# Kernel optimization log

Hardware: AMD Instinct MI355X
Metric: run time of the kernel (lower is better)

The kernel has to match this reference:

```python
import jax, jax.numpy as jnp
import numpy as np

BN_EPS = 1e-5
SQ_EPS = 1e-7
NUM_SAMPLES = 4
NUM_CHILD = 8
DIM_CHILD = 8
NUM_PARENT = 8
DIM_PARENT = 16
ROUTING_ITERS = 3
OFFSET_SCALE = 1.0


def squash(x, axis=-1):
    sq = jnp.sum(x * x, axis=axis, keepdims=True)
    return (sq / (1.0 + sq)) * x / jnp.sqrt(sq + SQ_EPS)


def bilinear_sample(feat, grid):
    # feat: [B,C,H,W], grid: [B,H,W,2] in [-1,1], align_corners=True, zeros padding
    B, C, H, W = feat.shape
    x = (grid[..., 0] + 1.0) * 0.5 * (W - 1)
    y = (grid[..., 1] + 1.0) * 0.5 * (H - 1)
    x0 = jnp.floor(x); y0 = jnp.floor(y)
    x1 = x0 + 1.0; y1 = y0 + 1.0
    wx1 = x - x0; wx0 = 1.0 - wx1
    wy1 = y - y0; wy0 = 1.0 - wy1
    featf = feat.reshape(B, C, H * W)

    def gather(xi, yi):
        valid = (xi >= 0) & (xi <= W - 1) & (yi >= 0) & (yi <= H - 1)
        xc = jnp.clip(xi, 0, W - 1).astype(jnp.int32)
        yc = jnp.clip(yi, 0, H - 1).astype(jnp.int32)
        idx = (yc * W + xc).reshape(B, 1, H * W)
        v = jnp.take_along_axis(featf, idx, axis=2).reshape(B, C, H, W)
        return v * valid[:, None].astype(feat.dtype)

    out = (gather(x0, y0) * (wx0 * wy0)[:, None]
           + gather(x1, y0) * (wx1 * wy0)[:, None]
           + gather(x0, y1) * (wx0 * wy1)[:, None]
           + gather(x1, y1) * (wx1 * wy1)[:, None])
    return out


def setup_inputs() -> dict:
    key = jax.random.key(0)
    ks = jax.random.split(key, 8)
    B, C, H, W = 8, 256, 32, 32
    caps_ch = NUM_CHILD * DIM_CHILD  # 64
    return {
        "x": jax.random.normal(ks[0], (B, C, H, W), jnp.float32),
        "primary_w": jax.random.normal(ks[1], (caps_ch, C), jnp.float32) * 0.05,
        "bn_gamma": jnp.ones((caps_ch,), jnp.float32),
        "bn_beta": jnp.zeros((caps_ch,), jnp.float32),
        "bn_mean": jax.random.normal(ks[2], (caps_ch,), jnp.float32) * 0.1,
        "bn_var": jax.random.uniform(ks[3], (caps_ch,), jnp.float32, 0.5, 1.5),
        "offset_w": jax.random.normal(ks[4], (2 * NUM_SAMPLES, C, 3, 3), jnp.float32) * 0.01,
        "offset_b": jnp.zeros((2 * NUM_SAMPLES,), jnp.float32),
        "routing_W": jax.random.normal(ks[5], (NUM_SAMPLES * NUM_CHILD, NUM_PARENT, DIM_PARENT, DIM_CHILD), jnp.float32) * 0.01,
    }


def reference(x, primary_w, bn_gamma, bn_beta, bn_mean, bn_var, offset_w, offset_b, routing_W):
    B, C, H, W = x.shape
    # --- PrimaryCaps: 1x1 conv + BN(inference) + SiLU + squash over capsule dim ---
    p = jnp.einsum('bchw,oc->bohw', x, primary_w)
    p = (p - bn_mean[None, :, None, None]) / jnp.sqrt(bn_var + BN_EPS)[None, :, None, None]
    p = p * bn_gamma[None, :, None, None] + bn_beta[None, :, None, None]
    p = jax.nn.silu(p)
    child = p.reshape(B, NUM_CHILD, DIM_CHILD, H, W)
    child = squash(child, axis=2)
    child_flat = child.reshape(B, NUM_CHILD * DIM_CHILD, H, W)

    # --- Offset conv 3x3, SAME padding ---
    off = jax.lax.conv_general_dilated(x, offset_w, (1, 1), 'SAME',
                                       dimension_numbers=('NCHW', 'OIHW', 'NCHW'))
    off = off + offset_b[None, :, None, None]
    off = off.reshape(B, NUM_SAMPLES, 2, H, W)
    off = jnp.tanh(off) * OFFSET_SCALE
    scale = jnp.array([max(W - 1, 1) / 2.0, max(H - 1, 1) / 2.0], x.dtype).reshape(1, 1, 2, 1, 1)
    off = off / scale

    ys = jnp.linspace(-1.0, 1.0, H, dtype=x.dtype)
    xs = jnp.linspace(-1.0, 1.0, W, dtype=x.dtype)
    yy, xx = jnp.meshgrid(ys, xs, indexing='ij')
    base = jnp.stack((xx, yy), axis=-1)  # [H,W,2]
    grids = base[None, None] + jnp.transpose(off, (0, 1, 3, 4, 2))  # [B,S,H,W,2]

    sampled = jax.vmap(lambda g: bilinear_sample(child_flat, g),
                       in_axes=1, out_axes=1)(grids)  # [B,S,caps_ch,H,W]
    sampled = sampled.reshape(B, NUM_SAMPLES, NUM_CHILD, DIM_CHILD, H, W)
    sampled = jnp.transpose(sampled, (0, 4, 5, 1, 2, 3))  # [B,H,W,S,NC,DC]
    sampled = sampled.reshape(B * H * W, NUM_SAMPLES * NUM_CHILD, DIM_CHILD)

    # --- Dynamic routing ---
    # u_hat: [M, N_in, N_out, D_out]
    u_hat = jnp.einsum('nodi,mni->mnod', routing_W, sampled)
    M = u_hat.shape[0]
    b = jnp.zeros((M, NUM_SAMPLES * NUM_CHILD, NUM_PARENT), x.dtype)
    v = None
    for it in range(ROUTING_ITERS):
        c = jax.nn.softmax(b, axis=-1)
        s = jnp.einsum('mno,mnod->mod', c, u_hat)
        v = squash(s, axis=-1)
        if it < ROUTING_ITERS - 1:
            b = b + jnp.einsum('mnod,mod->mno', u_hat, v)

    routed = v.reshape(B, H, W, NUM_PARENT, DIM_PARENT)
    out = jnp.transpose(routed, (0, 3, 4, 1, 2)).reshape(B, NUM_PARENT * DIM_PARENT, H, W)
    return out
```

## Files before the change

kernel.cpp:

```cpp
#include <hip/hip_runtime.h>
#include <math.h>

#define HW 1024
#define Hd 32
#define Wd 32
#define Bn 8
#define Cc 256

typedef _Float16 half2_t __attribute__((ext_vector_type(2)));
union F2H { float f; half2_t h; };

static __device__ __forceinline__ float dot2(half2_t a, half2_t b, float c) {
#if __has_builtin(__builtin_amdgcn_fdot2)
    return __builtin_amdgcn_fdot2(a, b, c, false);
#else
    return c + (float)a.x * (float)b.x + (float)a.y * (float)b.y;
#endif
}

template<int CTRL>
static __device__ __forceinline__ float dppx(float v) {
    union { float f; int i; } a, r;
    a.f = v;
    r.i = __builtin_amdgcn_update_dpp(0, a.i, CTRL, 0xF, 0xF, true);
    return r.f;
}

__global__ __launch_bounds__(256) void kTP(const float* __restrict__ x,
        const float* __restrict__ ow, const float* __restrict__ rw,
        float* __restrict__ xt, float* __restrict__ wt2,
        _Float16* __restrict__ wth) {
    __shared__ float tile[64][65];
    int bid = blockIdx.x;
    if (bid < 512) {
        int b = bid >> 6, ct = (bid >> 4) & 3, ht = bid & 15;
        int c0 = ct * 64, hw0 = ht * 64;
        int tr = threadIdx.x >> 6, tc = threadIdx.x & 63;
        const float* xb = x + ((size_t)b * 256 + c0) * 1024 + hw0;
        #pragma unroll
        for (int k = 0; k < 16; ++k) {
            int c = tr + k * 4;
            tile[c][tc] = xb[(size_t)c * 1024 + tc];
        }
        __syncthreads();
        float* xo = xt + ((size_t)b * 1024 + hw0) * 256 + c0;
        #pragma unroll
        for (int k = 0; k < 16; ++k) {
            int hwl = tr + k * 4;
            xo[(size_t)hwl * 256 + tc] = tile[tc][hwl];
        }
    } else if (bid < 584) {
        int t = (bid - 512) * 256 + threadIdx.x;
        int c = t & 255, oc = (t >> 8) & 7, tap = t >> 11;
        wt2[t] = ow[(oc * 256 + c) * 9 + tap];
    } else {
        int t = (bid - 584) * 256 + threadIdx.x;
        int i = t & 7, l = (t >> 3) & 63, j = t >> 9;
        int n = (l & 3) | ((l >> 1) & 0x1C);
        int half = (l >> 2) & 1;
        int o = j >> 4, d = j & 15;
        wth[t] = (_Float16)rw[n * 1024 + half * 512 + o * 128 + d * 8 + i];
    }
}

__global__ __launch_bounds__(256, 3) void kAB(const float* __restrict__ xt,
        const float* __restrict__ pw, const float* __restrict__ gamma,
        const float* __restrict__ beta, const float* __restrict__ mean,
        const float* __restrict__ var, const float* __restrict__ wt2,
        const float* __restrict__ ob, float* __restrict__ child_t,
        float* __restrict__ grids) {
    __shared__ float wl[16384];
    int wid = threadIdx.x >> 6, lane = threadIdx.x & 63;

    if (blockIdx.x < 512) {
        {
            const float4* pw4 = reinterpret_cast<const float4*>(pw);
            #pragma unroll
            for (int k = 0; k < 16; ++k) {
                int f = k * 256 + threadIdx.x;
                float4 v = pw4[f];
                int o = f >> 6, c4 = f & 63;
                *reinterpret_cast<float4*>(
                    wl + c4 * 256 + (((o ^ c4) & 63) << 2)) = v;
            }
        }
        __syncthreads();
        int o = lane;
        float scale = gamma[o] * rsqrtf(var[o] + 1e-5f);
        float mn = mean[o], bt = beta[o];
        const float4* wl4 = reinterpret_cast<const float4*>(wl);
        #pragma unroll
        for (int pp = 0; pp < 4; pp += 2) {
            int m0 = (blockIdx.x * 4 + wid) * 4 + pp;
            const float4* xa = reinterpret_cast<const float4*>(xt + (size_t)m0 * 256);
            const float4* xb = reinterpret_cast<const float4*>(xt + (size_t)(m0 + 1) * 256);
            float a0 = 0.f, a1 = 0.f;
            #pragma unroll 8
            for (int c4 = 0; c4 < 64; ++c4) {
                float4 wv = wl4[c4 * 64 + (lane ^ (c4 & 63))];
                float4 v0 = xa[c4], v1 = xb[c4];
                a0 += wv.x * v0.x + wv.y * v0.y + wv.z * v0.z + wv.w * v0.w;
                a1 += wv.x * v1.x + wv.y * v1.y + wv.z * v1.z + wv.w * v1.w;
            }
            #pragma unroll
            for (int e = 0; e < 2; ++e) {
                float acc = e ? a1 : a0;
                float t = (acc - mn) * scale + bt;
                float s = t / (1.f + expf(-t));
                float sq = s * s;
                sq += __shfl_xor(sq, 1);
                sq += __shfl_xor(sq, 2);
                sq += __shfl_xor(sq, 4);
                float f = (sq / (1.f + sq)) * rsqrtf(sq + 1e-7f);
                child_t[(size_t)(m0 + e) * 64 + o] = s * f;
            }
        }
        return;
    }

    {
        const float4* wt24 = reinterpret_cast<const float4*>(wt2);
        float4* wl4w = reinterpret_cast<float4*>(wl);
        #pragma unroll
        for (int k = 0; k < 16; ++k)
            wl4w[k * 256 + threadIdx.x] = wt24[k * 256 + threadIdx.x];
    }
    __syncthreads();

    int m0 = ((blockIdx.x - 512) * 4 + wid) * 4;
    int b = m0 >> 10, hw0 = m0 & 1023;
    int yy = hw0 >> 5, xx0 = hw0 & 31;
    const float* xb = xt + (size_t)b * HW * 256;

    float acc[4][8];
    #pragma unroll
    for (int px = 0; px < 4; ++px)
        #pragma unroll
        for (int oc = 0; oc < 8; ++oc) acc[px][oc] = 0.f;

    #pragma unroll
    for (int tap = 0; tap < 9; ++tap) {
        int ky = tap / 3 - 1, kx = tap % 3 - 1;
        int yq = yy + ky;
        bool vy = (yq >= 0) && (yq <= Hd - 1);
        float4 xv[4];
        #pragma unroll
        for (int px = 0; px < 4; ++px) {
            int xq = xx0 + px + kx;
            bool ok = vy && (xq >= 0) && (xq <= Wd - 1);
            float4 z; z.x = z.y = z.z = z.w = 0.f;
            xv[px] = ok ? *reinterpret_cast<const float4*>(
                              xb + (size_t)(yq * Wd + xq) * 256 + lane * 4)
                        : z;
        }
        #pragma unroll
        for (int oc = 0; oc < 8; ++oc) {
            float4 wv = (tap < 8)
                ? *reinterpret_cast<const float4*>(wl + (tap * 8 + oc) * 256 + lane * 4)
                : *reinterpret_cast<const float4*>(wt2 + (8 * 8 + oc) * 256 + lane * 4);
            #pragma unroll
            for (int px = 0; px < 4; ++px)
                acc[px][oc] += xv[px].x * wv.x + xv[px].y * wv.y +
                               xv[px].z * wv.z + xv[px].w * wv.w;
        }
    }

    int l0 = lane & 1, l1 = (lane >> 1) & 1;
    int o2 = (lane >> 2) & 1, o3 = (lane >> 3) & 1, o4 = (lane >> 4) & 1;
    float y1[2][8];
    #pragma unroll
    for (int ph = 0; ph < 2; ++ph)
        #pragma unroll
        for (int oc = 0; oc < 8; ++oc) {
            float keep = l0 ? acc[(ph << 1) | 1][oc] : acc[(ph << 1) | 0][oc];
            float send = l0 ? acc[(ph << 1) | 0][oc] : acc[(ph << 1) | 1][oc];
            y1[ph][oc] = keep + dppx<0xB1>(send);
        }
    float y2[8];
    #pragma unroll
    for (int oc = 0; oc < 8; ++oc) {
        float keep = l1 ? y1[1][oc] : y1[0][oc];
        float send = l1 ? y1[0][oc] : y1[1][oc];
        y2[oc] = keep + dppx<0x4E>(send);
    }
    float z4[4];
    #pragma unroll
    for (int oh = 0; oh < 4; ++oh) {
        float keep = o2 ? y2[(oh << 1) | 1] : y2[(oh << 1) | 0];
        float send = o2 ? y2[(oh << 1) | 0] : y2[(oh << 1) | 1];
        z4[oh] = keep + __shfl_xor(send, 4);
    }
    float w2[2];
    #pragma unroll
    for (int oh = 0; oh < 2; ++oh) {
        float keep = o3 ? z4[(oh << 1) | 1] : z4[(oh << 1) | 0];
        float send = o3 ? z4[(oh << 1) | 0] : z4[(oh << 1) | 1];
        w2[oh] = keep + dppx<0x128>(send);
    }
    {
        float keep = o4 ? w2[1] : w2[0];
        float send = o4 ? w2[0] : w2[1];
        float s = keep + __shfl_xor(send, 16);
        s += __shfl_xor(s, 32);
        if (lane < 32) {
            int px = lane & 3, oc = (lane >> 2) & 7;
            float t = tanhf(s + ob[oc]);
            int coord = oc & 1, si = oc >> 1;
            int xx = xx0 + px;
            float base = coord ? (-1.f + yy * (2.f / 31.f))
                               : (-1.f + xx * (2.f / 31.f));
            grids[(size_t)(m0 + px) * 8 + si * 2 + coord] =
                base + t * (1.f / 15.5f);
        }
    }
}

__global__ __launch_bounds__(64, 3) void kD(const float* __restrict__ child_t,
        const float* __restrict__ grids, const _Float16* __restrict__ wth,
        float* __restrict__ out) {
    __shared__ float vband[128];
    int lane = threadIdx.x & 63;
    int m = blockIdx.x;
    int b = m >> 10, hw = m & 1023;
    int n = (lane & 3) | ((lane >> 1) & 0x1C);
    int half = (lane >> 2) & 1;
    int si = n >> 3, ch = n & 7;
    int dsl = (n & 1) * 8 + ((n >> 1) & 1) * 4 + ((n >> 2) & 1) * 2 + ((n >> 3) & 1);

    float gx = grids[m * 8 + si * 2 + 0];
    float gy = grids[m * 8 + si * 2 + 1];
    float xf = (gx + 1.f) * 0.5f * 31.f;
    float yf = (gy + 1.f) * 0.5f * 31.f;
    float x0 = floorf(xf), y0 = floorf(yf);
    float wx1 = xf - x0, wx0 = 1.f - wx1;
    float wy1 = yf - y0, wy0 = 1.f - wy1;
    float sf[8] = {0.f, 0.f, 0.f, 0.f, 0.f, 0.f, 0.f, 0.f};
    const float* cb = child_t + (size_t)b * HW * 64 + ch * 8;
    #pragma unroll
    for (int cy = 0; cy < 2; ++cy) {
        float yq = y0 + (float)cy;
        bool vy = (yq >= 0.f) && (yq <= 31.f);
        float wy = cy ? wy1 : wy0;
        #pragma unroll
        for (int cx = 0; cx < 2; ++cx) {
            float xq = x0 + (float)cx;
            bool ok = vy && (xq >= 0.f) && (xq <= 31.f);
            if (!ok) continue;
            float w = wy * (cx ? wx1 : wx0);
            const float* cp = cb + (size_t)((int)yq * Wd + (int)xq) * 64;
            float4 v0 = *reinterpret_cast<const float4*>(cp);
            float4 v1 = *reinterpret_cast<const float4*>(cp + 4);
            sf[0] += w * v0.x; sf[1] += w * v0.y;
            sf[2] += w * v0.z; sf[3] += w * v0.w;
            sf[4] += w * v1.x; sf[5] += w * v1.y;
            sf[6] += w * v1.z; sf[7] += w * v1.w;
        }
    }
    half2_t sh0 = {(_Float16)sf[0], (_Float16)sf[1]};
    half2_t sh1 = {(_Float16)sf[2], (_Float16)sf[3]};
    half2_t sh2 = {(_Float16)sf[4], (_Float16)sf[5]};
    half2_t sh3 = {(_Float16)sf[6], (_Float16)sf[7]};

    float u[4][16];
    const float4* wt4 = reinterpret_cast<const float4*>(wth);
    #pragma unroll
    for (int o = 0; o < 4; ++o) {
        #pragma unroll
        for (int d = 0; d < 16; ++d) {
            float4 wv = wt4[(o * 16 + d) * 64 + lane];
            F2H a0, a1, a2, a3;
            a0.f = wv.x; a1.f = wv.y; a2.f = wv.z; a3.f = wv.w;
            float acc = dot2(a0.h, sh0, 0.f);
            acc = dot2(a1.h, sh1, acc);
            acc = dot2(a2.h, sh2, acc);
            acc = dot2(a3.h, sh3, acc);
            u[o][d] = acc;
        }
    }

    float bl[4] = {0.f, 0.f, 0.f, 0.f};
    #pragma unroll
    for (int it = 0; it < 3; ++it) {
        float ex[4], rs;
        if (it == 0) {
            ex[0] = ex[1] = ex[2] = ex[3] = 1.f;
            rs = 0.125f;
        } else {
            float mx = fmaxf(fmaxf(bl[0], bl[1]), fmaxf(bl[2], bl[3]));
            mx = fmaxf(mx, __shfl_xor(mx, 4));
            float ssum = 0.f;
            #pragma unroll
            for (int k = 0; k < 4; ++k) { ex[k] = expf(bl[k] - mx); ssum += ex[k]; }
            ssum += __shfl_xor(ssum, 4);
            rs = 1.f / ssum;
        }

        float sval[4];
        #pragma unroll
        for (int o = 0; o < 4; ++o) {
            float cc = ex[o] * rs;
            float y[8];
            #pragma unroll
            for (int d = 0; d < 8; ++d) {
                float t = (n & 1) ? cc * u[o][d] : cc * u[o][d + 8];
                float k = (n & 1) ? cc * u[o][d + 8] : cc * u[o][d];
                y[d] = k + dppx<0xB1>(t);
            }
            float z[4];
            #pragma unroll
            for (int d = 0; d < 4; ++d) {
                float t = (n & 2) ? y[d] : y[d + 4];
                float k = (n & 2) ? y[d + 4] : y[d];
                z[d] = k + dppx<0x4E>(t);
            }
            float w2[2];
            #pragma unroll
            for (int d = 0; d < 2; ++d) {
                float t = (n & 4) ? z[d] : z[d + 2];
                float k = (n & 4) ? z[d + 2] : z[d];
                w2[d] = k + dppx<0x128>(t);
            }
            float t4 = (n & 8) ? w2[0] : w2[1];
            float k4 = (n & 8) ? w2[1] : w2[0];
            float s1 = k4 + __shfl_xor(t4, 16);
            s1 += __shfl_xor(s1, 32);
            sval[o] = s1;
        }
        #pragma unroll
        for (int o = 0; o < 4; ++o) {
            float q = sval[o] * sval[o];
            q += dppx<0xB1>(q);
            q += dppx<0x4E>(q);
            q += dppx<0x128>(q);
            q += __shfl_xor(q, 16);
            float f = (q / (1.f + q)) / sqrtf(q + 1e-7f);
            if ((lane & 32) == 0)
                vband[(half * 4 + o) * 16 + dsl] = sval[o] * f;
        }
        if (it < 2) {
            #pragma unroll
            for (int o = 0; o < 4; ++o) {
                const float4* vr = reinterpret_cast<const float4*>(
                    vband + (half * 4 + o) * 16);
                float4 v0 = vr[0], v1 = vr[1], v2 = vr[2], v3 = vr[3];
                float agg = u[o][0] * v0.x + u[o][1] * v0.y +
                            u[o][2] * v0.z + u[o][3] * v0.w +
                            u[o][4] * v1.x + u[o][5] * v1.y +
                            u[o][6] * v1.z + u[o][7] * v1.w +
                            u[o][8] * v2.x + u[o][9] * v2.y +
                            u[o][10] * v2.z + u[o][11] * v2.w +
                            u[o][12] * v3.x + u[o][13] * v3.y +
                            u[o][14] * v3.z + u[o][15] * v3.w;
                bl[o] += agg;
            }
        } else {
            int o_own = lane >> 4;
            int och = half * 4 + o_own;
            int d0 = ((lane & 3) | ((lane >> 1) & 4)) * 2;
            float va = vband[och * 16 + d0 + 0];
            float vb = vband[och * 16 + d0 + 1];
            float* op = out + ((size_t)b * 128 + och * 16) * HW + hw;
            op[(size_t)(d0 + 0) * HW] = va;
            op[(size_t)(d0 + 1) * HW] = vb;
        }
    }
}

extern "C" void kernel_launch(void* const* d_in, const int* in_sizes, int n_in,
                              void* d_out, int out_size, void* d_ws, size_t ws_size,
                              hipStream_t stream) {
    const float* x     = (const float*)d_in[0];
    const float* pw    = (const float*)d_in[1];
    const float* gamma = (const float*)d_in[2];
    const float* beta  = (const float*)d_in[3];
    const float* mean  = (const float*)d_in[4];
    const float* var   = (const float*)d_in[5];
    const float* ow    = (const float*)d_in[6];
    const float* ob    = (const float*)d_in[7];
    const float* rw    = (const float*)d_in[8];
    float* out = (float*)d_out;
    char* ws = (char*)d_ws;
    float*     child_t = (float*)ws;
    float*     grids   = (float*)(ws + 2097152);
    _Float16*  wth     = (_Float16*)(ws + 2359296);
    float*     wt2     = (float*)(ws + 2424832);
    float*     xt      = (float*)(ws + 2498560);

    hipLaunchKernelGGL(kTP, dim3(712), dim3(256), 0, stream,
                       x, ow, rw, xt, wt2, wth);
    hipLaunchKernelGGL(kAB, dim3(1024), dim3(256), 0, stream,
                       xt, pw, gamma, beta, mean, var, wt2, ob,
                       child_t, grids);
    hipLaunchKernelGGL(kD, dim3(8192), dim3(64), 0, stream,
                       child_t, grids, wth, out);
}
```

Measured before the change: 85.52 us.

## Restructure routing kernel to four waves over two pixels with one parent per lane

The routing kernel now runs 256-thread blocks that each handle two pixels. Every wave owns two parent capsules, and each lane holds u_hat for one child and one parent across both pixels. Bilinear samples are computed once per block and shared through LDS. The softmax over parents is exchanged through an LDS table, which needs extra block barriers. The aim is to reuse each routing-weight load across two pixels and cut per-lane register pressure, paid for with more __syncthreads per routing iteration and a reordered weight layout.

```diff
diff --git a/kernel.cpp b/kernel.cpp
--- a/kernel.cpp
+++ b/kernel.cpp
@@ -55,11 +55,10 @@
         wt2[t] = ow[(oc * 256 + c) * 9 + tap];
     } else {
         int t = (bid - 584) * 256 + threadIdx.x;
-        int i = t & 7, l = (t >> 3) & 63, j = t >> 9;
-        int n = (l & 3) | ((l >> 1) & 0x1C);
-        int half = (l >> 2) & 1;
-        int o = j >> 4, d = j & 15;
-        wth[t] = (_Float16)rw[n * 1024 + half * 512 + o * 128 + d * 8 + i];
+        int i = t & 7, l = (t >> 3) & 63, j = (t >> 9) & 15, w = t >> 13;
+        int n = l & 31, s = l >> 5;
+        int o = 2 * w + s;
+        wth[t] = (_Float16)rw[n * 1024 + o * 128 + j * 8 + i];
     }
 }
 
@@ -215,95 +214,139 @@
     }
 }
 
-__global__ __launch_bounds__(64, 3) void kD(const float* __restrict__ child_t,
+__global__ __launch_bounds__(256, 2) void kD(const float* __restrict__ child_t,
         const float* __restrict__ grids, const _Float16* __restrict__ wth,
         float* __restrict__ out) {
-    __shared__ float vband[128];
-    int lane = threadIdx.x & 63;
-    int m = blockIdx.x;
-    int b = m >> 10, hw = m & 1023;
-    int n = (lane & 3) | ((lane >> 1) & 0x1C);
-    int half = (lane >> 2) & 1;
-    int si = n >> 3, ch = n & 7;
+    __shared__ float smp[2][32][8];
+    __shared__ float btab[2][32][8];
+    __shared__ float vband[2][8][16];
+    int tid = threadIdx.x;
+    int w = tid >> 6, lane = tid & 63;
+    int n = lane & 31, sh = lane >> 5;
+    int o_own = 2 * w + sh;
     int dsl = (n & 1) * 8 + ((n >> 1) & 1) * 4 + ((n >> 2) & 1) * 2 + ((n >> 3) & 1);
-
-    float gx = grids[m * 8 + si * 2 + 0];
-    float gy = grids[m * 8 + si * 2 + 1];
-    float xf = (gx + 1.f) * 0.5f * 31.f;
-    float yf = (gy + 1.f) * 0.5f * 31.f;
-    float x0 = floorf(xf), y0 = floorf(yf);
-    float wx1 = xf - x0, wx0 = 1.f - wx1;
-    float wy1 = yf - y0, wy0 = 1.f - wy1;
-    float sf[8] = {0.f, 0.f, 0.f, 0.f, 0.f, 0.f, 0.f, 0.f};
-    const float* cb = child_t + (size_t)b * HW * 64 + ch * 8;
-    #pragma unroll
-    for (int cy = 0; cy < 2; ++cy) {
-        float yq = y0 + (float)cy;
-        bool vy = (yq >= 0.f) && (yq <= 31.f);
-        float wy = cy ? wy1 : wy0;
-        #pragma unroll
-        for (int cx = 0; cx < 2; ++cx) {
-            float xq = x0 + (float)cx;
-            bool ok = vy && (xq >= 0.f) && (xq <= 31.f);
-            if (!ok) continue;
-            float w = wy * (cx ? wx1 : wx0);
-            const float* cp = cb + (size_t)((int)yq * Wd + (int)xq) * 64;
-            float4 v0 = *reinterpret_cast<const float4*>(cp);
-            float4 v1 = *reinterpret_cast<const float4*>(cp + 4);
-            sf[0] += w * v0.x; sf[1] += w * v0.y;
-            sf[2] += w * v0.z; sf[3] += w * v0.w;
-            sf[4] += w * v1.x; sf[5] += w * v1.y;
-            sf[6] += w * v1.z; sf[7] += w * v1.w;
-        }
-    }
-    half2_t sh0 = {(_Float16)sf[0], (_Float16)sf[1]};
-    half2_t sh1 = {(_Float16)sf[2], (_Float16)sf[3]};
-    half2_t sh2 = {(_Float16)sf[4], (_Float16)sf[5]};
-    half2_t sh3 = {(_Float16)sf[6], (_Float16)sf[7]};
-
-    float u[4][16];
-    const float4* wt4 = reinterpret_cast<const float4*>(wth);
-    #pragma unroll
-    for (int o = 0; o < 4; ++o) {
-        #pragma unroll
-        for (int d = 0; d < 16; ++d) {
-            float4 wv = wt4[(o * 16 + d) * 64 + lane];
-            F2H a0, a1, a2, a3;
-            a0.f = wv.x; a1.f = wv.y; a2.f = wv.z; a3.f = wv.w;
-            float acc = dot2(a0.h, sh0, 0.f);
-            acc = dot2(a1.h, sh1, acc);
-            acc = dot2(a2.h, sh2, acc);
-            acc = dot2(a3.h, sh3, acc);
-            u[o][d] = acc;
-        }
-    }
-
-    float bl[4] = {0.f, 0.f, 0.f, 0.f};
+    int mA = blockIdx.x * 2;
+    int bA_ = mA >> 10, hwA = mA & 1023;
+    int bB_ = (mA + 1) >> 10, hwB = (mA + 1) & 1023;
+
+    if (tid < 64) {
+        int px = tid >> 5, ns = tid & 31;
+        int sis = ns >> 3, chs = ns & 7;
+        int m = mA + px;
+        int b = m >> 10;
+        float gx = grids[m * 8 + sis * 2 + 0];
+        float gy = grids[m * 8 + sis * 2 + 1];
+        float xf = (gx + 1.f) * 0.5f * 31.f;
+        float yf = (gy + 1.f) * 0.5f * 31.f;
+        float x0 = floorf(xf), y0 = floorf(yf);
+        float wx1 = xf - x0, wx0 = 1.f - wx1;
+        float wy1 = yf - y0, wy0 = 1.f - wy1;
+        float sf[8] = {0.f, 0.f, 0.f, 0.f, 0.f, 0.f, 0.f, 0.f};
+        const float* cb = child_t + (size_t)b * HW * 64 + chs * 8;
+        #pragma unroll
+        for (int cy = 0; cy < 2; ++cy) {
+            float yq = y0 + (float)cy;
+            bool vy = (yq >= 0.f) && (yq <= 31.f);
+            float wy = cy ? wy1 : wy0;
+            #pragma unroll
+            for (int cx = 0; cx < 2; ++cx) {
+                float xq = x0 + (float)cx;
+                bool ok = vy && (xq >= 0.f) && (xq <= 31.f);
+                if (!ok) continue;
+                float wgt = wy * (cx ? wx1 : wx0);
+                const float* cp = cb + (size_t)((int)yq * Wd + (int)xq) * 64;
+                float4 v0 = *reinterpret_cast<const float4*>(cp);
+                float4 v1 = *reinterpret_cast<const float4*>(cp + 4);
+                sf[0] += wgt * v0.x; sf[1] += wgt * v0.y;
+                sf[2] += wgt * v0.z; sf[3] += wgt * v0.w;
+                sf[4] += wgt * v1.x; sf[5] += wgt * v1.y;
+                sf[6] += wgt * v1.z; sf[7] += wgt * v1.w;
+            }
+        }
+        float4 s0; s0.x = sf[0]; s0.y = sf[1]; s0.z = sf[2]; s0.w = sf[3];
+        float4 s1; s1.x = sf[4]; s1.y = sf[5]; s1.z = sf[6]; s1.w = sf[7];
+        reinterpret_cast<float4*>(&smp[px][ns][0])[0] = s0;
+        reinterpret_cast<float4*>(&smp[px][ns][0])[1] = s1;
+    }
+    __syncthreads();
+
+    half2_t sha[4], shb[4];
+    {
+        const float4* pa = reinterpret_cast<const float4*>(&smp[0][n][0]);
+        float4 a0 = pa[0], a1 = pa[1];
+        sha[0] = half2_t{(_Float16)a0.x, (_Float16)a0.y};
+        sha[1] = half2_t{(_Float16)a0.z, (_Float16)a0.w};
+        sha[2] = half2_t{(_Float16)a1.x, (_Float16)a1.y};
+        sha[3] = half2_t{(_Float16)a1.z, (_Float16)a1.w};
+        const float4* pb = reinterpret_cast<const float4*>(&smp[1][n][0]);
+        float4 b0 = pb[0], b1 = pb[1];
+        shb[0] = half2_t{(_Float16)b0.x, (_Float16)b0.y};
+        shb[1] = half2_t{(_Float16)b0.z, (_Float16)b0.w};
+        shb[2] = half2_t{(_Float16)b1.x, (_Float16)b1.y};
+        shb[3] = half2_t{(_Float16)b1.z, (_Float16)b1.w};
+    }
+
+    float ua[16], ub[16];
+    const float4* wt4 = reinterpret_cast<const float4*>(wth) + (size_t)w * 16 * 64 + lane;
+    #pragma unroll
+    for (int j = 0; j < 16; ++j) {
+        float4 wv = wt4[j * 64];
+        F2H a0, a1, a2, a3;
+        a0.f = wv.x; a1.f = wv.y; a2.f = wv.z; a3.f = wv.w;
+        float acc = dot2(a0.h, sha[0], 0.f);
+        acc = dot2(a1.h, sha[1], acc);
+        acc = dot2(a2.h, sha[2], acc);
+        acc = dot2(a3.h, sha[3], acc);
+        ua[j] = acc;
+        float accB = dot2(a0.h, shb[0], 0.f);
+        accB = dot2(a1.h, shb[1], accB);
+        accB = dot2(a2.h, shb[2], accB);
+        accB = dot2(a3.h, shb[3], accB);
+        ub[j] = accB;
+    }
+
+    float bA = 0.f, bB = 0.f;
     #pragma unroll
     for (int it = 0; it < 3; ++it) {
-        float ex[4], rs;
+        float cA, cB;
         if (it == 0) {
-            ex[0] = ex[1] = ex[2] = ex[3] = 1.f;
-            rs = 0.125f;
+            cA = 0.125f; cB = 0.125f;
         } else {
-            float mx = fmaxf(fmaxf(bl[0], bl[1]), fmaxf(bl[2], bl[3]));
-            mx = fmaxf(mx, __shfl_xor(mx, 4));
-            float ssum = 0.f;
-            #pragma unroll
-            for (int k = 0; k < 4; ++k) { ex[k] = expf(bl[k] - mx); ssum += ex[k]; }
-            ssum += __shfl_xor(ssum, 4);
-            rs = 1.f / ssum;
-        }
-
-        float sval[4];
-        #pragma unroll
-        for (int o = 0; o < 4; ++o) {
-            float cc = ex[o] * rs;
+            __syncthreads();
+            btab[0][n][o_own] = bA;
+            btab[1][n][o_own] = bB;
+            __syncthreads();
+            float4 qa0 = reinterpret_cast<const float4*>(&btab[0][n][0])[0];
+            float4 qa1 = reinterpret_cast<const float4*>(&btab[0][n][0])[1];
+            float4 qb0 = reinterpret_cast<const float4*>(&btab[1][n][0])[0];
+            float4 qb1 = reinterpret_cast<const float4*>(&btab[1][n][0])[1];
+            float mxA = fmaxf(fmaxf(fmaxf(qa0.x, qa0.y), fmaxf(qa0.z, qa0.w)),
+                              fmaxf(fmaxf(qa1.x, qa1.y), fmaxf(qa1.z, qa1.w)));
+            float esA = expf(qa0.x - mxA) + expf(qa0.y - mxA) +
+                        expf(qa0.z - mxA) + expf(qa0.w - mxA) +
+                        expf(qa1.x - mxA) + expf(qa1.y - mxA) +
+                        expf(qa1.z - mxA) + expf(qa1.w - mxA);
+            cA = expf(bA - mxA) / esA;
+            float mxB = fmaxf(fmaxf(fmaxf(qb0.x, qb0.y), fmaxf(qb0.z, qb0.w)),
+                              fmaxf(fmaxf(qb1.x, qb1.y), fmaxf(qb1.z, qb1.w)));
+            float esB = expf(qb0.x - mxB) + expf(qb0.y - mxB) +
+                        expf(qb0.z - mxB) + expf(qb0.w - mxB) +
+                        expf(qb1.x - mxB) + expf(qb1.y - mxB) +
+                        expf(qb1.z - mxB) + expf(qb1.w - mxB);
+            cB = expf(bB - mxB) / esB;
+        }
+
+        #pragma unroll
+        for (int px = 0; px < 2; ++px) {
+            float cc = px ? cB : cA;
+            float sp[16];
+            #pragma unroll
+            for (int j = 0; j < 16; ++j) sp[j] = cc * (px ? ub[j] : ua[j]);
             float y[8];
             #pragma unroll
             for (int d = 0; d < 8; ++d) {
-                float t = (n & 1) ? cc * u[o][d] : cc * u[o][d + 8];
-                float k = (n & 1) ? cc * u[o][d + 8] : cc * u[o][d];
+                float t = (n & 1) ? sp[d] : sp[d + 8];
+                float k = (n & 1) ? sp[d + 8] : sp[d];
                 y[d] = k + dppx<0xB1>(t);
             }
             float z[4];
@@ -318,50 +361,41 @@
             for (int d = 0; d < 2; ++d) {
                 float t = (n & 4) ? z[d] : z[d + 2];
                 float k = (n & 4) ? z[d + 2] : z[d];
-                w2[d] = k + dppx<0x128>(t);
+                w2[d] = k + __shfl_xor(t, 4);
             }
             float t4 = (n & 8) ? w2[0] : w2[1];
             float k4 = (n & 8) ? w2[1] : w2[0];
-            float s1 = k4 + __shfl_xor(t4, 16);
-            s1 += __shfl_xor(s1, 32);
-            sval[o] = s1;
-        }
-        #pragma unroll
-        for (int o = 0; o < 4; ++o) {
-            float q = sval[o] * sval[o];
+            float s1 = k4 + dppx<0x128>(t4);
+            s1 += __shfl_xor(s1, 16);
+            float q = s1 * s1;
             q += dppx<0xB1>(q);
             q += dppx<0x4E>(q);
+            q += __shfl_xor(q, 4);
             q += dppx<0x128>(q);
-            q += __shfl_xor(q, 16);
             float f = (q / (1.f + q)) / sqrtf(q + 1e-7f);
-            if ((lane & 32) == 0)
-                vband[(half * 4 + o) * 16 + dsl] = sval[o] * f;
-        }
-        if (it < 2) {
-            #pragma unroll
-            for (int o = 0; o < 4; ++o) {
+            float v = s1 * f;
+            if (it < 2) {
+                if (!(n & 16)) vband[px][o_own][dsl] = v;
                 const float4* vr = reinterpret_cast<const float4*>(
-                    vband + (half * 4 + o) * 16);
+                    &vband[px][o_own][0]);
                 float4 v0 = vr[0], v1 = vr[1], v2 = vr[2], v3 = vr[3];
-                float agg = u[o][0] * v0.x + u[o][1] * v0.y +
-                            u[o][2] * v0.z + u[o][3] * v0.w +
-                            u[o][4] * v1.x + u[o][5] * v1.y +
-                            u[o][6] * v1.z + u[o][7] * v1.w +
-                            u[o][8] * v2.x + u[o][9] * v2.y +
-                            u[o][10] * v2.z + u[o][11] * v2.w +
-                            u[o][12] * v3.x + u[o][13] * v3.y +
-                            u[o][14] * v3.z + u[o][15] * v3.w;
-                bl[o] += agg;
-            }
-        } else {
-            int o_own = lane >> 4;
-            int och = half * 4 + o_own;
-            int d0 = ((lane & 3) | ((lane >> 1) & 4)) * 2;
-            float va = vband[och * 16 + d0 + 0];
-            float vb = vband[och * 16 + d0 + 1];
-            float* op = out + ((size_t)b * 128 + och * 16) * HW + hw;
-            op[(size_t)(d0 + 0) * HW] = va;
-            op[(size_t)(d0 + 1) * HW] = vb;
+                const float* uu = px ? ub : ua;
+                float agg = uu[0] * v0.x + uu[1] * v0.y +
+                            uu[2] * v0.z + uu[3] * v0.w +
+                            uu[4] * v1.x + uu[5] * v1.y +
+                            uu[6] * v1.z + uu[7] * v1.w +
+                            uu[8] * v2.x + uu[9] * v2.y +
+                            uu[10] * v2.z + uu[11] * v2.w +
+                            uu[12] * v3.x + uu[13] * v3.y +
+                            uu[14] * v3.z + uu[15] * v3.w;
+                if (px) bB += agg; else bA += agg;
+            } else {
+                if (!(n & 16)) {
+                    int bo = px ? bB_ : bA_;
+                    int hwo = px ? hwB : hwA;
+                    out[((size_t)bo * 128 + o_own * 16 + dsl) * HW + hwo] = v;
+                }
+            }
         }
     }
 }
@@ -391,6 +425,6 @@
     hipLaunchKernelGGL(kAB, dim3(1024), dim3(256), 0, stream,
                        xt, pw, gamma, beta, mean, var, wt2, ob,
                        child_t, grids);
-    hipLaunchKernelGGL(kD, dim3(8192), dim3(64), 0, stream,
+    hipLaunchKernelGGL(kD, dim3(4096), dim3(256), 0, stream,
                        child_t, grids, wth, out);
 }
```

Result: slower. 97.66 us (+14.2%).
